# Kernel tuning notes

Hardware: AMD Instinct MI355X
Metric: run time of the kernel (lower is better)

Reference implementation:

```python
import jax, jax.numpy as jnp
import numpy as np

PI = 3.1415927410125732
N = 4096
VELOCITY = 5e-7
RC = 3.15e-6          # collision radius
RR = 8e-6             # repulsion radius
RO = 2.5e-5           # orientation radius (Ra = inf -> inside_Ra all-true)
ALPHA = PI            # field of view; < 2*pi so within_view masking is active
DT_TRANS = 1.4e-14    # translational diffusion DT
DR = 0.0028
GAMMA = 25.0
DT = 0.2              # timestep dt
COLLISION_ITERS = 3   # fixed-iteration version of recursive solve_collisions
EPS = 1e-14


def _c(x):  # [N,2] real -> complex64
    return jax.lax.complex(x[..., 0], x[..., 1])


def _r(z):  # complex -> [..., 2] real
    return jnp.stack([z.real, z.imag], axis=-1)


def _anglediff(a, b):
    # torch get_anglediff: wrap angle(a)-angle(b) into (-pi, pi)
    diff = jnp.angle(a) - jnp.angle(b)
    diff = jnp.where(diff <= -PI, jnp.mod(diff, PI), diff)
    return diff - (diff >= PI) * (2.0 * PI)


def _cossim(a, b):
    # nn.CosineSimilarity(dim=1, eps=1e-14) on view_as_real of complex vectors
    dot = a.real * b.real + a.imag * b.imag
    na = jnp.sqrt(a.real ** 2 + a.imag ** 2 + 1e-30)
    nb = jnp.sqrt(b.real ** 2 + b.imag ** 2 + 1e-30)
    return dot / (jnp.maximum(na, EPS) * jnp.maximum(nb, EPS))


def setup_inputs() -> dict:
    key = jax.random.key(0)
    k1, k2, k3, k4, k5 = jax.random.split(key, 5)
    positions = jax.random.normal(k1, (N, 2), jnp.float32) * 5e-4
    ang = jax.random.uniform(k2, (N,), jnp.float32, -PI, PI)
    orientations = jnp.stack([jnp.cos(ang), jnp.sin(ang)], axis=-1)  # unit complex
    Deltas = jax.random.uniform(k3, (1,), jnp.float32, 0.1, 0.6)
    rot_noise = jax.random.normal(k4, (N,), jnp.float32)
    trans_noise = jax.random.normal(k5, (N, 2), jnp.float32)
    return {"positions": positions, "orientations": orientations, "Deltas": Deltas,
            "rot_noise": rot_noise, "trans_noise": trans_noise}


def reference(positions, orientations, Deltas, rot_noise, trans_noise):
    p = _c(positions)      # [N] complex positions
    u = _c(orientations)   # [N] complex orientations
    n = p.shape[0]
    eye = jnp.eye(n, dtype=bool)

    # pairwise direction/distance: dirs[i,j] = p_j - p_i
    dirs = p[None, :] - p[:, None]
    dists = jnp.abs(dirs)

    inside_Rr = (dists <= RR) & ~eye
    inside_Ro = dists <= RO + RC
    # inside_Ra with Ra = inf is all-True

    # angle between separation vector and orientation of the *neighbor* j
    ang_diff = _anglediff(dirs, u[None, :])
    in_front = ang_diff < PI / 2
    within_view = ang_diff < ALPHA  # alpha < 2*pi branch active

    cdtype = p.dtype
    mask_rr = (inside_Rr & in_front).astype(cdtype)
    mask_ra = within_view.astype(cdtype)  # inside_Ra all True
    mask_ro = (inside_Ro & within_view).astype(cdtype)

    n_r = mask_rr.real.sum(axis=1)
    S = (mask_rr @ p) / jnp.maximum(n_r, 1.0) - p * jnp.sign(n_r)
    d = -S

    n_a = mask_ra.real.sum(axis=1)
    cms = (mask_ra @ p) / jnp.maximum(n_a, 1.0)
    Ps = cms - p * jnp.sign(n_a)

    orientation_sums = mask_ro @ u

    leftturns = Ps * jnp.exp(1j * Deltas)
    rightturns = Ps * jnp.exp(-1j * Deltas)

    # T >= T_release branch: pick the turn most aligned with neighbor orientations
    left_closer = _cossim(leftturns, orientation_sums) >= _cossim(rightturns, orientation_sums)
    best_turns = jnp.where(left_closer, leftturns, rightturns)

    d_abs = jnp.abs(d)
    d_safe = jnp.where(d_abs > 0, d, jnp.ones((), cdtype))
    best_safe = jnp.where(jnp.abs(best_turns) > 0, best_turns, jnp.ones((), cdtype))
    angle_to_target = jnp.where(d_abs > 0, _anglediff(d_safe, u), _anglediff(best_safe, u))

    # rotational_noise = randn * sqrt(2*DR); rotation = exp(i*(dt*Gamma*DR*sin + noise*sqrt(dt)))
    rot = jnp.exp(1j * (DT * GAMMA * DR * jnp.sin(angle_to_target)
                        + rot_noise * np.float32(np.sqrt(2 * DR)) * np.float32(np.sqrt(DT))))

    # complex-normal translational noise (per-component std 1/sqrt(2)) * sqrt(2*DT) * sqrt(dt)
    tn = _c(trans_noise) * np.float32(np.sqrt(0.5)) * np.float32(np.sqrt(2 * DT_TRANS))
    translation = DT * VELOCITY * u + tn * np.float32(np.sqrt(DT))

    def collide(i, pos):
        dd = pos[None, :] - pos[:, None]
        dd_nd = jnp.where(eye, jnp.ones((), pos.dtype), dd)  # avoid 0/0 on diagonal
        ab = jnp.where(eye, 0.0, jnp.abs(dd_nd))
        coll = ab <= 2 * RC - jnp.eye(n, dtype=ab.dtype)
        safe = jnp.where(coll, ab, 1.0)
        move = jnp.where(coll, dd / safe * ((2.1 * RC - ab) * 0.5), jnp.zeros((), pos.dtype))
        return pos - move.sum(axis=1)

    new_p = jax.lax.fori_loop(0, COLLISION_ITERS, collide, p + translation)
    new_u = u * rot

    # pack the 5 complex outputs as real [5, N, 2]
    return jnp.stack([_r(new_p), _r(new_u), _r(orientation_sums), _r(leftturns), _r(rightturns)], axis=0)
```

## Files before the change

kernel.cpp:

```cpp
#include <hip/hip_runtime.h>
#include <math.h>

#define NPART 4096
#define NBLK  512
#define NTHR  256
#define IPB   8
#define SMAX  256
#define GDIM  64
#define NCELL (GDIM * GDIM)
#define PPT   (NPART / NTHR)

constexpr float RORC   = (float)(2.5e-5 + 3.15e-6);
constexpr float RORC2  = RORC * RORC;
constexpr float RRF    = 8e-6f;
constexpr float RR2    = RRF * RRF;
constexpr float TWORC  = (float)(2.0 * 3.15e-6);
constexpr float TWORC2 = TWORC * TWORC;
constexpr float C21RC  = (float)(2.1 * 3.15e-6);
constexpr float RCAND2 = 1.6e-9f;
constexpr float GMIN   = -2.048e-3f;
constexpr float GINV   = 15625.0f;
constexpr float C_ROT  = (float)(0.2 * 25.0 * 0.0028);
constexpr float C_RN1  = (float)0.07483314773547883;
constexpr float C_SQDT = (float)0.4472135954999579;
constexpr float C_TRV  = (float)(0.2 * 5e-7);
constexpr float C_HALF = (float)0.7071067811865476;
constexpr float C_SQ2T = (float)1.6733200530681511e-07;
constexpr float EPSF   = 1e-14f;

__device__ __forceinline__ int cell_of(float x, float y) {
    int cx = (int)floorf((x - GMIN) * GINV);
    int cy = (int)floorf((y - GMIN) * GINV);
    cx = min(max(cx, 0), GDIM - 1);
    cy = min(max(cy, 0), GDIM - 1);
    return cy * GDIM + cx;
}

__global__ __launch_bounds__(NTHR) void fused_all(
        const float2* __restrict__ pos, const float2* __restrict__ ori,
        const float* __restrict__ Deltas, const float* __restrict__ rot_noise,
        const float2* __restrict__ trans_noise, float2* __restrict__ out) {
    __shared__ int      ptr[NCELL];
    __shared__ unsigned short sortid[NPART];
    __shared__ float4   sortpos4[NPART / 2];
    __shared__ float    sred[2 * NTHR];
    __shared__ float    res[5][IPB];
    __shared__ unsigned bmap[NPART / 32];
    __shared__ int      Sidx[SMAX];
    __shared__ float4   posS4[SMAX / 2];
    __shared__ int      scnt;
    float2* sortpos = (float2*)sortpos4;
    float2* posS    = (float2*)posS4;
    int*    sredi   = (int*)sred;

    const int tid  = threadIdx.x;
    const int il   = tid >> 5;
    const int lane = tid & 31;
    const int gi   = blockIdx.x * IPB + il;

    if (tid == 0) scnt = IPB;
    if (tid < IPB) Sidx[tid] = blockIdx.x * IPB + tid;
    if (tid < NPART / 32) bmap[tid] = 0u;
    for (int k = 0; k < NCELL / NTHR; ++k)
        ptr[k * NTHR + tid] = 0;

    float2 pp[PPT];
    int    cc[PPT];
    #pragma unroll
    for (int k = 0; k < PPT; ++k)
        pp[k] = pos[k * NTHR + tid];
    __syncthreads();
    #pragma unroll
    for (int k = 0; k < PPT; ++k) {
        cc[k] = cell_of(pp[k].x, pp[k].y);
        atomicAdd(&ptr[cc[k]], 1);
    }
    __syncthreads();

    {
        const int base = tid * (NCELL / NTHR);
        int v[NCELL / NTHR];
        int sum = 0;
        #pragma unroll
        for (int t = 0; t < NCELL / NTHR; ++t) { v[t] = ptr[base + t]; sum += v[t]; }
        sredi[tid] = sum;
        __syncthreads();
        for (int off = 1; off < NTHR; off <<= 1) {
            const int a = (tid >= off) ? sredi[tid - off] : 0;
            __syncthreads();
            sredi[tid] += a;
            __syncthreads();
        }
        int run = sredi[tid] - sum;
        #pragma unroll
        for (int t = 0; t < NCELL / NTHR; ++t) { ptr[base + t] = run; run += v[t]; }
    }
    __syncthreads();

    #pragma unroll
    for (int k = 0; k < PPT; ++k) {
        const int slot = atomicAdd(&ptr[cc[k]], 1);
        sortid[slot]  = (unsigned short)(k * NTHR + tid);
        sortpos[slot] = pp[k];
    }
    __syncthreads();

    const float2 pi = pos[gi];
    float nr = 0.f, sx = 0.f, sy = 0.f, oxs = 0.f, oys = 0.f;
    {
        int cxi = min(max((int)floorf((pi.x - GMIN) * GINV), 0), GDIM - 1);
        int cyi = min(max((int)floorf((pi.y - GMIN) * GINV), 0), GDIM - 1);
        for (int dyr = -1; dyr <= 1; ++dyr) {
            const int cy = cyi + dyr;
            if (cy < 0 || cy >= GDIM) continue;
            const int c_lo = cy * GDIM + max(cxi - 1, 0);
            const int c_hi = cy * GDIM + min(cxi + 1, GDIM - 1);
            const int b0 = (c_lo > 0) ? ptr[c_lo - 1] : 0;
            const int e0 = ptr[c_hi];
            for (int t = b0 + lane; t < e0; t += 32) {
                const float2 pj = sortpos[t];
                const float dxp = pj.x - pi.x, dyp = pj.y - pi.y;
                const float r2 = fmaf(dxp, dxp, dyp * dyp);
                if (r2 <= RCAND2) {
                    const int j = sortid[t];
                    atomicOr(&bmap[j >> 5], 1u << (j & 31));
                    if (r2 <= RORC2) {
                        const float2 uj = ori[j];
                        oxs += uj.x; oys += uj.y;
                        if (r2 <= RR2 && r2 > 0.f) {
                            const float dt_ = fmaf(dxp, uj.x, dyp * uj.y);
                            const float cr_ = fmaf(dyp, uj.x, -dxp * uj.y);
                            if (!((dt_ <= 0.f) && (cr_ >= 0.f))) {
                                nr += 1.f; sx += pj.x; sy += pj.y;
                            }
                        }
                    }
                }
            }
        }
    }
    {
        float vals[5] = {nr, sx, sy, oxs, oys};
        #pragma unroll
        for (int q = 0; q < 5; ++q)
            #pragma unroll
            for (int off = 16; off >= 1; off >>= 1)
                vals[q] += __shfl_down(vals[q], off, 32);
        if (lane == 0) {
            res[0][il] = vals[0]; res[1][il] = vals[1]; res[2][il] = vals[2];
            res[3][il] = vals[3]; res[4][il] = vals[4];
        }
    }
    __syncthreads();

    if (tid < NPART / 32) {
        unsigned bits = bmap[tid];
        if (tid == (int)(blockIdx.x >> 2))
            bits &= ~(0xFFu << ((blockIdx.x & 3) * 8));
        while (bits) {
            const int b = __ffs(bits) - 1;
            bits &= bits - 1;
            const int slot = atomicAdd(&scnt, 1);
            if (slot < SMAX) Sidx[slot] = tid * 32 + b;
        }
    }
    __syncthreads();
    const int nS = (scnt < SMAX) ? scnt : SMAX;

    if (tid < nS) {
        const int p = Sidx[tid];
        const float2 pq = pos[p];
        const float2 uu = ori[p];
        const float2 tn = trans_noise[p];
        posS[tid] = make_float2(
            pq.x + (C_TRV * uu.x + ((tn.x * C_HALF) * C_SQ2T) * C_SQDT),
            pq.y + (C_TRV * uu.y + ((tn.y * C_HALF) * C_SQ2T) * C_SQDT));
    }

    float mx = 0.f, my = 0.f;
    #pragma unroll
    for (int k = 0; k < PPT; ++k) { mx += pp[k].x; my += pp[k].y; }
    sred[tid] = mx; sred[NTHR + tid] = my;
    __syncthreads();
    for (int s = NTHR / 2; s > 0; s >>= 1) {
        if (tid < s) { sred[tid] += sred[tid + s]; sred[NTHR + tid] += sred[NTHR + tid + s]; }
        __syncthreads();
    }
    const float cmx = sred[0]    * (1.f / NPART);
    const float cmy = sred[NTHR] * (1.f / NPART);

    if (tid < IPB) {
        const int g2 = blockIdx.x * IPB + tid;
        const float2 p = pos[g2];
        const float2 u = ori[g2];
        const float nrv = res[0][tid], sxv = res[1][tid], syv = res[2][tid];
        const float osx = res[3][tid], osy = res[4][tid];

        const float inv = 1.f / fmaxf(nrv, 1.f);
        const float sg  = (nrv > 0.f) ? 1.f : 0.f;
        const float Sx = sxv * inv - p.x * sg;
        const float Sy = syv * inv - p.y * sg;
        const float dxv = -Sx, dyv = -Sy;

        const float Psx = cmx - p.x;
        const float Psy = cmy - p.y;

        float sd, cd;
        sincosf(Deltas[0], &sd, &cd);
        const float Lx = Psx * cd - Psy * sd;
        const float Ly = Psx * sd + Psy * cd;
        const float Rx = Psx * cd + Psy * sd;
        const float Ry = Psy * cd - Psx * sd;

        const float no  = fmaxf(sqrtf(osx * osx + osy * osy + 1e-30f), EPSF);
        const float nl  = fmaxf(sqrtf(Lx * Lx + Ly * Ly + 1e-30f), EPSF);
        const float nrr = fmaxf(sqrtf(Rx * Rx + Ry * Ry + 1e-30f), EPSF);
        const float csl = (Lx * osx + Ly * osy) / (nl * no);
        const float csr = (Rx * osx + Ry * osy) / (nrr * no);
        const bool left = (csl >= csr);
        const float bx = left ? Lx : Rx;
        const float by = left ? Ly : Ry;

        float cx, cy;
        if (dxv != 0.f || dyv != 0.f)    { cx = dxv; cy = dyv; }
        else if (bx != 0.f || by != 0.f) { cx = bx;  cy = by;  }
        else                             { cx = 1.f; cy = 0.f; }

        const float dt_ = cx * u.x + cy * u.y;
        const float cr_ = cy * u.x - cx * u.y;
        const float sin_t = cr_ / sqrtf(dt_ * dt_ + cr_ * cr_);

        const float ang = C_ROT * sin_t + (rot_noise[g2] * C_RN1) * C_SQDT;
        float sa, ca;
        sincosf(ang, &sa, &ca);
        out[1 * NPART + g2] = make_float2(u.x * ca - u.y * sa,
                                          u.x * sa + u.y * ca);
        out[2 * NPART + g2] = make_float2(osx, osy);
        out[3 * NPART + g2] = make_float2(Lx, Ly);
        out[4 * NPART + g2] = make_float2(Rx, Ry);
    }
    __syncthreads();

    for (int pass = 0; pass < 3; ++pass) {
        float px = 0.f, py = 0.f, ax = 0.f, ay = 0.f;
        const bool mv = (tid < nS);
        if (mv) { px = posS[tid].x; py = posS[tid].y; }
        int b = 0;
        for (; b + 4 <= nS; b += 4) {
            const float4 w0 = posS4[(b >> 1)];
            const float4 w1 = posS4[(b >> 1) + 1];
            const float bxs[4] = {w0.x, w0.z, w1.x, w1.z};
            const float bys[4] = {w0.y, w0.w, w1.y, w1.w};
            #pragma unroll
            for (int s = 0; s < 4; ++s) {
                if (mv) {
                    const float dx = bxs[s] - px, dy = bys[s] - py;
                    const float r2 = fmaf(dx, dx, dy * dy);
                    if (r2 <= TWORC2 && r2 > 0.f) {
                        const float ab = sqrtf(r2);
                        const float sc = (C21RC - ab) * 0.5f / ab;
                        ax = fmaf(dx, sc, ax);
                        ay = fmaf(dy, sc, ay);
                    }
                }
            }
        }
        for (; b < nS; ++b) {
            const float2 pb = posS[b];
            if (mv) {
                const float dx = pb.x - px, dy = pb.y - py;
                const float r2 = fmaf(dx, dx, dy * dy);
                if (r2 <= TWORC2 && r2 > 0.f) {
                    const float ab = sqrtf(r2);
                    const float sc = (C21RC - ab) * 0.5f / ab;
                    ax = fmaf(dx, sc, ax);
                    ay = fmaf(dy, sc, ay);
                }
            }
        }
        __syncthreads();
        if (mv) posS[tid] = make_float2(px - ax, py - ay);
        __syncthreads();
    }
    if (tid < IPB)
        out[0 * NPART + blockIdx.x * IPB + tid] = posS[tid];
}

extern "C" void kernel_launch(void* const* d_in, const int* in_sizes, int n_in,
                              void* d_out, int out_size, void* d_ws, size_t ws_size,
                              hipStream_t stream) {
    const float2* pos = (const float2*)d_in[0];
    const float2* ori = (const float2*)d_in[1];
    const float*  del = (const float*)d_in[2];
    const float*  rn  = (const float*)d_in[3];
    const float2* tn  = (const float2*)d_in[4];
    float2* o2 = (float2*)d_out;
    (void)d_ws; (void)ws_size;

    fused_all<<<dim3(NBLK), dim3(NTHR), 0, stream>>>(pos, ori, del, rn, tn, o2);
}
```

Baseline: 89.20 us.

## Replace per-block cell-list sort with brute-force neighbor scan over all particles

Removes the per-block spatial grid build (atomic histogram, block-wide prefix scan, scatter sort). Each 64-lane wavefront now linearly scans all 4096 positions staged in LDS to find neighbours, so every particle is tested against every other. Blocks are halved to 4 particles each and doubled in count, and the launch bounds ask for higher occupancy. This drops several barriers and shared-memory atomics, but the distance checks per block grow from a few cells' worth to the full particle set.

```diff
diff --git a/kernel.cpp b/kernel.cpp
--- a/kernel.cpp
+++ b/kernel.cpp
@@ -2,12 +2,10 @@
 #include <math.h>
 
 #define NPART 4096
-#define NBLK  512
+#define NBLK  1024
 #define NTHR  256
-#define IPB   8
+#define IPB   4
 #define SMAX  256
-#define GDIM  64
-#define NCELL (GDIM * GDIM)
 #define PPT   (NPART / NTHR)
 
 constexpr float RORC   = (float)(2.5e-5 + 3.15e-6);
@@ -18,8 +16,6 @@
 constexpr float TWORC2 = TWORC * TWORC;
 constexpr float C21RC  = (float)(2.1 * 3.15e-6);
 constexpr float RCAND2 = 1.6e-9f;
-constexpr float GMIN   = -2.048e-3f;
-constexpr float GINV   = 15625.0f;
 constexpr float C_ROT  = (float)(0.2 * 25.0 * 0.0028);
 constexpr float C_RN1  = (float)0.07483314773547883;
 constexpr float C_SQDT = (float)0.4472135954999579;
@@ -28,112 +24,74 @@
 constexpr float C_SQ2T = (float)1.6733200530681511e-07;
 constexpr float EPSF   = 1e-14f;
 
-__device__ __forceinline__ int cell_of(float x, float y) {
-    int cx = (int)floorf((x - GMIN) * GINV);
-    int cy = (int)floorf((y - GMIN) * GINV);
-    cx = min(max(cx, 0), GDIM - 1);
-    cy = min(max(cy, 0), GDIM - 1);
-    return cy * GDIM + cx;
-}
-
-__global__ __launch_bounds__(NTHR) void fused_all(
+__global__ __launch_bounds__(NTHR, 4) void fused_all(
         const float2* __restrict__ pos, const float2* __restrict__ ori,
         const float* __restrict__ Deltas, const float* __restrict__ rot_noise,
         const float2* __restrict__ trans_noise, float2* __restrict__ out) {
-    __shared__ int      ptr[NCELL];
-    __shared__ unsigned short sortid[NPART];
-    __shared__ float4   sortpos4[NPART / 2];
+    __shared__ float4   posL4[NPART / 2];
     __shared__ float    sred[2 * NTHR];
     __shared__ float    res[5][IPB];
     __shared__ unsigned bmap[NPART / 32];
     __shared__ int      Sidx[SMAX];
     __shared__ float4   posS4[SMAX / 2];
     __shared__ int      scnt;
-    float2* sortpos = (float2*)sortpos4;
-    float2* posS    = (float2*)posS4;
-    int*    sredi   = (int*)sred;
+    float2* posL = (float2*)posL4;
+    float2* posS = (float2*)posS4;
 
     const int tid  = threadIdx.x;
-    const int il   = tid >> 5;
-    const int lane = tid & 31;
+    const int il   = tid >> 6;
+    const int lane = tid & 63;
     const int gi   = blockIdx.x * IPB + il;
 
     if (tid == 0) scnt = IPB;
     if (tid < IPB) Sidx[tid] = blockIdx.x * IPB + tid;
     if (tid < NPART / 32) bmap[tid] = 0u;
-    for (int k = 0; k < NCELL / NTHR; ++k)
-        ptr[k * NTHR + tid] = 0;
-
-    float2 pp[PPT];
-    int    cc[PPT];
-    #pragma unroll
-    for (int k = 0; k < PPT; ++k)
-        pp[k] = pos[k * NTHR + tid];
-    __syncthreads();
+
+    float mx = 0.f, my = 0.f;
     #pragma unroll
     for (int k = 0; k < PPT; ++k) {
-        cc[k] = cell_of(pp[k].x, pp[k].y);
-        atomicAdd(&ptr[cc[k]], 1);
-    }
-    __syncthreads();
-
-    {
-        const int base = tid * (NCELL / NTHR);
-        int v[NCELL / NTHR];
-        int sum = 0;
-        #pragma unroll
-        for (int t = 0; t < NCELL / NTHR; ++t) { v[t] = ptr[base + t]; sum += v[t]; }
-        sredi[tid] = sum;
-        __syncthreads();
-        for (int off = 1; off < NTHR; off <<= 1) {
-            const int a = (tid >= off) ? sredi[tid - off] : 0;
-            __syncthreads();
-            sredi[tid] += a;
-            __syncthreads();
-        }
-        int run = sredi[tid] - sum;
-        #pragma unroll
-        for (int t = 0; t < NCELL / NTHR; ++t) { ptr[base + t] = run; run += v[t]; }
-    }
-    __syncthreads();
-
-    #pragma unroll
-    for (int k = 0; k < PPT; ++k) {
-        const int slot = atomicAdd(&ptr[cc[k]], 1);
-        sortid[slot]  = (unsigned short)(k * NTHR + tid);
-        sortpos[slot] = pp[k];
-    }
-    __syncthreads();
-
-    const float2 pi = pos[gi];
+        const float2 v = pos[k * NTHR + tid];
+        posL[k * NTHR + tid] = v;
+        mx += v.x; my += v.y;
+    }
+    sred[tid] = mx; sred[NTHR + tid] = my;
+    __syncthreads();
+
+    const float2 pi = posL[gi];
     float nr = 0.f, sx = 0.f, sy = 0.f, oxs = 0.f, oys = 0.f;
-    {
-        int cxi = min(max((int)floorf((pi.x - GMIN) * GINV), 0), GDIM - 1);
-        int cyi = min(max((int)floorf((pi.y - GMIN) * GINV), 0), GDIM - 1);
-        for (int dyr = -1; dyr <= 1; ++dyr) {
-            const int cy = cyi + dyr;
-            if (cy < 0 || cy >= GDIM) continue;
-            const int c_lo = cy * GDIM + max(cxi - 1, 0);
-            const int c_hi = cy * GDIM + min(cxi + 1, GDIM - 1);
-            const int b0 = (c_lo > 0) ? ptr[c_lo - 1] : 0;
-            const int e0 = ptr[c_hi];
-            for (int t = b0 + lane; t < e0; t += 32) {
-                const float2 pj = sortpos[t];
-                const float dxp = pj.x - pi.x, dyp = pj.y - pi.y;
-                const float r2 = fmaf(dxp, dxp, dyp * dyp);
-                if (r2 <= RCAND2) {
-                    const int j = sortid[t];
-                    atomicOr(&bmap[j >> 5], 1u << (j & 31));
-                    if (r2 <= RORC2) {
-                        const float2 uj = ori[j];
-                        oxs += uj.x; oys += uj.y;
-                        if (r2 <= RR2 && r2 > 0.f) {
-                            const float dt_ = fmaf(dxp, uj.x, dyp * uj.y);
-                            const float cr_ = fmaf(dyp, uj.x, -dxp * uj.y);
-                            if (!((dt_ <= 0.f) && (cr_ >= 0.f))) {
-                                nr += 1.f; sx += pj.x; sy += pj.y;
-                            }
-                        }
+    #pragma unroll 2
+    for (int t = lane; t < NPART / 2; t += 64) {
+        const float4 w = posL4[t];
+        const float dx0 = w.x - pi.x, dy0 = w.y - pi.y;
+        const float r20 = fmaf(dx0, dx0, dy0 * dy0);
+        const float dx1 = w.z - pi.x, dy1 = w.w - pi.y;
+        const float r21 = fmaf(dx1, dx1, dy1 * dy1);
+        if (r20 <= RCAND2) {
+            const int j = 2 * t;
+            atomicOr(&bmap[j >> 5], 1u << (j & 31));
+            if (r20 <= RORC2) {
+                const float2 uj = ori[j];
+                oxs += uj.x; oys += uj.y;
+                if (r20 <= RR2 && r20 > 0.f) {
+                    const float dt_ = fmaf(dx0, uj.x, dy0 * uj.y);
+                    const float cr_ = fmaf(dy0, uj.x, -dx0 * uj.y);
+                    if (!((dt_ <= 0.f) && (cr_ >= 0.f))) {
+                        nr += 1.f; sx += w.x; sy += w.y;
+                    }
+                }
+            }
+        }
+        if (r21 <= RCAND2) {
+            const int j = 2 * t + 1;
+            atomicOr(&bmap[j >> 5], 1u << (j & 31));
+            if (r21 <= RORC2) {
+                const float2 uj = ori[j];
+                oxs += uj.x; oys += uj.y;
+                if (r21 <= RR2 && r21 > 0.f) {
+                    const float dt_ = fmaf(dx1, uj.x, dy1 * uj.y);
+                    const float cr_ = fmaf(dy1, uj.x, -dx1 * uj.y);
+                    if (!((dt_ <= 0.f) && (cr_ >= 0.f))) {
+                        nr += 1.f; sx += w.z; sy += w.w;
                     }
                 }
             }
@@ -144,8 +102,8 @@
         #pragma unroll
         for (int q = 0; q < 5; ++q)
             #pragma unroll
-            for (int off = 16; off >= 1; off >>= 1)
-                vals[q] += __shfl_down(vals[q], off, 32);
+            for (int off = 32; off >= 1; off >>= 1)
+                vals[q] += __shfl_down(vals[q], off);
         if (lane == 0) {
             res[0][il] = vals[0]; res[1][il] = vals[1]; res[2][il] = vals[2];
             res[3][il] = vals[3]; res[4][il] = vals[4];
@@ -155,8 +113,8 @@
 
     if (tid < NPART / 32) {
         unsigned bits = bmap[tid];
-        if (tid == (int)(blockIdx.x >> 2))
-            bits &= ~(0xFFu << ((blockIdx.x & 3) * 8));
+        if (tid == (int)(blockIdx.x >> 3))
+            bits &= ~(0xFu << ((blockIdx.x & 7) * 4));
         while (bits) {
             const int b = __ffs(bits) - 1;
             bits &= bits - 1;
@@ -169,7 +127,7 @@
 
     if (tid < nS) {
         const int p = Sidx[tid];
-        const float2 pq = pos[p];
+        const float2 pq = posL[p];
         const float2 uu = ori[p];
         const float2 tn = trans_noise[p];
         posS[tid] = make_float2(
@@ -177,11 +135,6 @@
             pq.y + (C_TRV * uu.y + ((tn.y * C_HALF) * C_SQ2T) * C_SQDT));
     }
 
-    float mx = 0.f, my = 0.f;
-    #pragma unroll
-    for (int k = 0; k < PPT; ++k) { mx += pp[k].x; my += pp[k].y; }
-    sred[tid] = mx; sred[NTHR + tid] = my;
-    __syncthreads();
     for (int s = NTHR / 2; s > 0; s >>= 1) {
         if (tid < s) { sred[tid] += sred[tid + s]; sred[NTHR + tid] += sred[NTHR + tid + s]; }
         __syncthreads();
@@ -191,7 +144,7 @@
 
     if (tid < IPB) {
         const int g2 = blockIdx.x * IPB + tid;
-        const float2 p = pos[g2];
+        const float2 p = posL[g2];
         const float2 u = ori[g2];
         const float nrv = res[0][tid], sxv = res[1][tid], syv = res[2][tid];
         const float osx = res[3][tid], osy = res[4][tid];
```

Result: faster. 82.87 us (-7.1%).
